# Optimization experiments

Hardware: AMD Instinct MI355X
Metric: run time of the kernel (lower is better)

The kernel has to match this reference:

```python
import jax, jax.numpy as jnp
import numpy as np

B, L, H, E = 8, 4096, 8, 64
NEIGH = 128          # neigh_size: local window length (entries per row of band mask)
SPLITS = 32          # number of Q blocks
L1 = L // SPLITS     # rows per block = 128 (neigh_size <= L/splits holds with equality)


def setup_inputs() -> dict:
    key = jax.random.key(0)
    kq, kk, kv = jax.random.split(key, 3)
    return {
        "queries": jax.random.normal(kq, (B, L, H, E), jnp.float32),
        "keys":    jax.random.normal(kk, (B, L, H, E), jnp.float32),
        "values":  jax.random.normal(kv, (B, L, H, E), jnp.float32),
    }


def reference(queries, keys, values):
    scale = 1.0 / np.sqrt(E)
    # Global key index of each entry in a KV block: block j covers [j*l1 - neigh, j*l1 + l1)
    kv_idx = (jnp.arange(SPLITS)[:, None] * L1
              + jnp.arange(L1 + NEIGH)[None, :] - NEIGH)      # [splits, l1+neigh]
    kv_gather = jnp.clip(kv_idx, 0, L - 1)                    # out-of-range entries get masked

    Qb = queries.reshape(B, SPLITS, L1, H, E)                 # [B, j, l, H, E]
    Kb = keys[:, kv_gather]                                   # [B, j, m, H, E]
    Vb = values[:, kv_gather]                                 # [B, j, m, H, E]

    scores = jnp.einsum('bjlhe,bjmhe->bhjlm', Qb, Kb) * scale # [B, H, splits, l1, l1+neigh]

    # Band: key global index k satisfies q - neigh < k <= q  <=>  l < m <= l + neigh
    l_idx = jnp.arange(L1)[:, None]
    m_idx = jnp.arange(L1 + NEIGH)[None, :]
    band = (m_idx > l_idx) & (m_idx <= l_idx + NEIGH)         # [l1, l1+neigh]
    valid = band[None, :, :] & (kv_idx[:, None, :] >= 0)      # [splits, l1, l1+neigh]

    scores = jnp.where(valid[None, None], scores, jnp.float32(-1e9))
    attn = jax.nn.softmax(scores, axis=-1)
    out = jnp.einsum('bhjlm,bjmhe->bjlhe', attn, Vb)          # [B, splits, l1, H, E]
    return out.reshape(B, L, H, E)
```

## Files before the change

kernel.cpp:

```cpp
#include <hip/hip_runtime.h>

#define B_ 8
#define L_ 4096
#define H_ 8
#define E_ 64
#define NEIGH_ 128
#define SPLITS_ 32
#define BQ 128
#define WIN 256
#define KPAD 72
#define NT 10
#define NP 5

typedef float f32x4 __attribute__((ext_vector_type(4)));
typedef __bf16 bf16x8 __attribute__((ext_vector_type(8)));
typedef unsigned short u16x4 __attribute__((ext_vector_type(4)));
typedef unsigned short u16x8 __attribute__((ext_vector_type(8)));
typedef unsigned int u32;

__device__ inline unsigned short f2bf(float f) {
  unsigned int u = __float_as_uint(f);
  u += 0x7fff + ((u >> 16) & 1);
  return (unsigned short)(u >> 16);
}
__device__ inline u32 pack2(float a, float b) {
  return (u32)f2bf(a) | ((u32)f2bf(b) << 16);
}

__global__ __launch_bounds__(512, 4) void la_kernel(
    const float* __restrict__ Q, const float* __restrict__ K,
    const float* __restrict__ V, float* __restrict__ out) {
  const int lid = blockIdx.x + SPLITS_ * (blockIdx.y + H_ * blockIdx.z);
  const int logical = (lid & 7) * 256 + (lid >> 3);
  const int j = logical & (SPLITS_ - 1);
  const int h = (logical >> 5) & (H_ - 1);
  const int b = logical >> 8;
  const int t = threadIdx.x;

  __shared__ unsigned short Ks[WIN * KPAD];
  __shared__ u32 Vs32[E_ * (WIN / 2)];

  const int q0 = j * BQ;
  const int g0 = q0 - NEIGH_;

  for (int i = 0; i < 8; ++i) {
    int idx = t + i * 512;
    int km = idx >> 4, c4 = idx & 15;
    int g = g0 + km; g = g < 0 ? 0 : g;
    const float4 v = *(const float4*)(K + ((((size_t)b * L_) + g) * H_ + h) * E_ + c4 * 4);
    u16x4 p = { f2bf(v.x), f2bf(v.y), f2bf(v.z), f2bf(v.w) };
    *(u16x4*)&Ks[km * KPAD + c4 * 4] = p;
  }
  for (int i = 0; i < 4; ++i) {
    int idx = t + i * 512;
    int kp = idx >> 4, c4 = idx & 15;
    int k0g = g0 + 2 * kp, k1g = k0g + 1;
    k0g = k0g < 0 ? 0 : k0g; k1g = k1g < 0 ? 0 : k1g;
    const float4 v0 = *(const float4*)(V + ((((size_t)b * L_) + k0g) * H_ + h) * E_ + c4 * 4);
    const float4 v1 = *(const float4*)(V + ((((size_t)b * L_) + k1g) * H_ + h) * E_ + c4 * 4);
    int g = kp >> 2;
    int ko = kp & 3;
    const float a0[4] = {v0.x, v0.y, v0.z, v0.w};
    const float a1[4] = {v1.x, v1.y, v1.z, v1.w};
#pragma unroll
    for (int w = 0; w < 4; ++w) {
      int e = c4 * 4 + w;
      int gs = g ^ (e & 31);
      Vs32[e * 128 + gs * 4 + ko] = pack2(a0[w], a1[w]);
    }
  }

  const int wv = t >> 6, lane = t & 63;
  const int l15 = lane & 15, quad = lane >> 4;
  const int r0 = wv * 16;
  const int lq = r0 + l15;
  const int start = wv & ~1;
  const int ks0 = start >> 1;

  bf16x8 qfrag[2];
  {
    const float* qrow = Q + ((((size_t)b * L_) + q0 + lq) * H_ + h) * E_;
#pragma unroll
    for (int ks = 0; ks < 2; ++ks) {
      const float4 x = *(const float4*)(qrow + ks * 32 + quad * 8);
      const float4 y = *(const float4*)(qrow + ks * 32 + quad * 8 + 4);
      u16x8 p = { f2bf(x.x), f2bf(x.y), f2bf(x.z), f2bf(x.w),
                  f2bf(y.x), f2bf(y.y), f2bf(y.z), f2bf(y.w) };
      qfrag[ks] = __builtin_bit_cast(bf16x8, p);
    }
  }
  __syncthreads();

  f32x4 S[NT];
#pragma unroll
  for (int si = 0; si < NT; ++si) S[si] = (f32x4){0.f, 0.f, 0.f, 0.f};
#pragma unroll
  for (int ks = 0; ks < 2; ++ks) {
#pragma unroll
    for (int si = 0; si < NT; ++si) {
      int kt = start + si;
      bf16x8 a = __builtin_bit_cast(bf16x8,
          *(const u16x8*)&Ks[(kt * 16 + l15) * KPAD + ks * 32 + quad * 8]);
      S[si] = __builtin_amdgcn_mfma_f32_16x16x32_bf16(a, qfrag[ks], S[si], 0, 0, 0);
    }
  }

  float m = -1e30f;
#pragma unroll
  for (int si = 0; si < NT; ++si) {
#pragma unroll
    for (int r = 0; r < 4; ++r) {
      int key = (start + si) * 16 + quad * 4 + r;
      float s = S[si][r] * 0.125f;
      bool valid = (key > lq) & (key <= lq + NEIGH_) & (g0 + key >= 0);
      s = valid ? s : -1e30f;
      S[si][r] = s;
      m = fmaxf(m, s);
    }
  }
  m = fmaxf(m, __shfl_xor(m, 16));
  m = fmaxf(m, __shfl_xor(m, 32));

  float lsum = 0.f;
  u32 pk[NT][2];
#pragma unroll
  for (int si = 0; si < NT; ++si) {
    float p0 = __expf(S[si][0] - m);
    float p1 = __expf(S[si][1] - m);
    float p2 = __expf(S[si][2] - m);
    float p3 = __expf(S[si][3] - m);
    lsum += (p0 + p1) + (p2 + p3);
    pk[si][0] = pack2(p0, p1);
    pk[si][1] = pack2(p2, p3);
  }
  lsum += __shfl_xor(lsum, 16);
  lsum += __shfl_xor(lsum, 32);
  const float inv = 1.0f / lsum;

  f32x4 O[4];
#pragma unroll
  for (int et = 0; et < 4; ++et) O[et] = (f32x4){0.f, 0.f, 0.f, 0.f};
  const int srcBase = 16 * ((quad & 1) * 2) + l15;
  const bool hiTile = (quad >> 1) != 0;
#pragma unroll
  for (int pi = 0; pi < NP; ++pi) {
    const int ap = ks0 + pi;
    u32 a32[4];
#pragma unroll
    for (int k = 0; k < 4; ++k) {
      int src = srcBase + 16 * (k >> 1);
      u32 u0 = (u32)__shfl((int)pk[2 * pi][k & 1], src);
      u32 u1 = (u32)__shfl((int)pk[2 * pi + 1][k & 1], src);
      a32[k] = hiTile ? u1 : u0;
    }
    bf16x8 afrag = __builtin_bit_cast(bf16x8,
        (u32 __attribute__((ext_vector_type(4)))){a32[0], a32[1], a32[2], a32[3]});
#pragma unroll
    for (int et = 0; et < 4; ++et) {
      int e = et * 16 + l15;
      int gs = (ap * 4 + quad) ^ (e & 31);
      bf16x8 bfrag = __builtin_bit_cast(bf16x8,
          *(const u16x8*)((const unsigned short*)Vs32 + e * 256 + gs * 8));
      O[et] = __builtin_amdgcn_mfma_f32_16x16x32_bf16(afrag, bfrag, O[et], 0, 0, 0);
    }
  }

  float invq[4];
#pragma unroll
  for (int r = 0; r < 4; ++r) invq[r] = __shfl(inv, quad * 4 + r);
#pragma unroll
  for (int et = 0; et < 4; ++et)
#pragma unroll
    for (int r = 0; r < 4; ++r) {
      int row = r0 + quad * 4 + r;
      out[((((size_t)b * L_) + q0 + row) * H_ + h) * E_ + et * 16 + l15] = O[et][r] * invq[r];
    }
}

extern "C" void kernel_launch(void* const* d_in, const int* in_sizes, int n_in,
                              void* d_out, int out_size, void* d_ws, size_t ws_size,
                              hipStream_t stream) {
  const float* q = (const float*)d_in[0];
  const float* k = (const float*)d_in[1];
  const float* v = (const float*)d_in[2];
  float* o = (float*)d_out;
  dim3 grid(SPLITS_, H_, B_);
  la_kernel<<<grid, 512, 0, stream>>>(q, k, v, o);
}
```

Before: 226.1 us.

## Load K fragments directly from global memory and drop K shared-memory staging

K is no longer staged in LDS. Each wave loads its own K rows from global memory straight into MFMA fragments, which removes the K LDS write/read and moves the barrier to after the softmax so the V staging overlaps with QK compute. It also switches to native bf16 conversion intrinsics, raises the launch-bounds occupancy hint from 4 to 6, and raises wave priority around the PV MFMAs. In exchange, K is read redundantly from global (overlapping windows across waves, via L2) and register pressure may spill under the tighter launch bound.

```diff
diff --git a/kernel.cpp b/kernel.cpp
--- a/kernel.cpp
+++ b/kernel.cpp
@@ -8,26 +8,27 @@
 #define SPLITS_ 32
 #define BQ 128
 #define WIN 256
-#define KPAD 72
 #define NT 10
 #define NP 5
 
 typedef float f32x4 __attribute__((ext_vector_type(4)));
+typedef __bf16 bf16x2 __attribute__((ext_vector_type(2)));
 typedef __bf16 bf16x8 __attribute__((ext_vector_type(8)));
-typedef unsigned short u16x4 __attribute__((ext_vector_type(4)));
 typedef unsigned short u16x8 __attribute__((ext_vector_type(8)));
 typedef unsigned int u32;
+typedef u32 u32x4 __attribute__((ext_vector_type(4)));
 
-__device__ inline unsigned short f2bf(float f) {
-  unsigned int u = __float_as_uint(f);
-  u += 0x7fff + ((u >> 16) & 1);
-  return (unsigned short)(u >> 16);
+__device__ inline u32 pack2(float a, float b) {
+  bf16x2 t = {(__bf16)a, (__bf16)b};
+  return __builtin_bit_cast(u32, t);
 }
-__device__ inline u32 pack2(float a, float b) {
-  return (u32)f2bf(a) | ((u32)f2bf(b) << 16);
+__device__ inline bf16x8 cvt8(const float4& x, const float4& y) {
+  bf16x8 r = {(__bf16)x.x, (__bf16)x.y, (__bf16)x.z, (__bf16)x.w,
+              (__bf16)y.x, (__bf16)y.y, (__bf16)y.z, (__bf16)y.w};
+  return r;
 }
 
-__global__ __launch_bounds__(512, 4) void la_kernel(
+__global__ __launch_bounds__(512, 6) void la_kernel(
     const float* __restrict__ Q, const float* __restrict__ K,
     const float* __restrict__ V, float* __restrict__ out) {
   const int lid = blockIdx.x + SPLITS_ * (blockIdx.y + H_ * blockIdx.z);
@@ -37,20 +38,11 @@
   const int b = logical >> 8;
   const int t = threadIdx.x;
 
-  __shared__ unsigned short Ks[WIN * KPAD];
   __shared__ u32 Vs32[E_ * (WIN / 2)];
 
   const int q0 = j * BQ;
   const int g0 = q0 - NEIGH_;
 
-  for (int i = 0; i < 8; ++i) {
-    int idx = t + i * 512;
-    int km = idx >> 4, c4 = idx & 15;
-    int g = g0 + km; g = g < 0 ? 0 : g;
-    const float4 v = *(const float4*)(K + ((((size_t)b * L_) + g) * H_ + h) * E_ + c4 * 4);
-    u16x4 p = { f2bf(v.x), f2bf(v.y), f2bf(v.z), f2bf(v.w) };
-    *(u16x4*)&Ks[km * KPAD + c4 * 4] = p;
-  }
   for (int i = 0; i < 4; ++i) {
     int idx = t + i * 512;
     int kp = idx >> 4, c4 = idx & 15;
@@ -84,25 +76,24 @@
     for (int ks = 0; ks < 2; ++ks) {
       const float4 x = *(const float4*)(qrow + ks * 32 + quad * 8);
       const float4 y = *(const float4*)(qrow + ks * 32 + quad * 8 + 4);
-      u16x8 p = { f2bf(x.x), f2bf(x.y), f2bf(x.z), f2bf(x.w),
-                  f2bf(y.x), f2bf(y.y), f2bf(y.z), f2bf(y.w) };
-      qfrag[ks] = __builtin_bit_cast(bf16x8, p);
+      qfrag[ks] = cvt8(x, y);
     }
   }
-  __syncthreads();
 
   f32x4 S[NT];
 #pragma unroll
   for (int si = 0; si < NT; ++si) S[si] = (f32x4){0.f, 0.f, 0.f, 0.f};
 #pragma unroll
-  for (int ks = 0; ks < 2; ++ks) {
-#pragma unroll
-    for (int si = 0; si < NT; ++si) {
-      int kt = start + si;
-      bf16x8 a = __builtin_bit_cast(bf16x8,
-          *(const u16x8*)&Ks[(kt * 16 + l15) * KPAD + ks * 32 + quad * 8]);
-      S[si] = __builtin_amdgcn_mfma_f32_16x16x32_bf16(a, qfrag[ks], S[si], 0, 0, 0);
-    }
+  for (int si = 0; si < NT; ++si) {
+    int g = g0 + (start + si) * 16 + l15;
+    g = g < 0 ? 0 : g;
+    const float* krow = K + ((((size_t)b * L_) + g) * H_ + h) * E_;
+    const float4 x0 = *(const float4*)(krow + quad * 8);
+    const float4 y0 = *(const float4*)(krow + quad * 8 + 4);
+    const float4 x1 = *(const float4*)(krow + 32 + quad * 8);
+    const float4 y1 = *(const float4*)(krow + 32 + quad * 8 + 4);
+    S[si] = __builtin_amdgcn_mfma_f32_16x16x32_bf16(cvt8(x0, y0), qfrag[0], S[si], 0, 0, 0);
+    S[si] = __builtin_amdgcn_mfma_f32_16x16x32_bf16(cvt8(x1, y1), qfrag[1], S[si], 0, 0, 0);
   }
 
   float m = -1e30f;
@@ -137,6 +128,8 @@
   lsum += __shfl_xor(lsum, 32);
   const float inv = 1.0f / lsum;
 
+  __syncthreads();
+
   f32x4 O[4];
 #pragma unroll
   for (int et = 0; et < 4; ++et) O[et] = (f32x4){0.f, 0.f, 0.f, 0.f};
@@ -154,7 +147,8 @@
       a32[k] = hiTile ? u1 : u0;
     }
     bf16x8 afrag = __builtin_bit_cast(bf16x8,
-        (u32 __attribute__((ext_vector_type(4)))){a32[0], a32[1], a32[2], a32[3]});
+        (u32x4){a32[0], a32[1], a32[2], a32[3]});
+    __builtin_amdgcn_s_setprio(1);
 #pragma unroll
     for (int et = 0; et < 4; ++et) {
       int e = et * 16 + l15;
@@ -163,6 +157,7 @@
           *(const u16x8*)((const unsigned short*)Vs32 + e * 256 + gs * 8));
       O[et] = __builtin_amdgcn_mfma_f32_16x16x32_bf16(afrag, bfrag, O[et], 0, 0, 0);
     }
+    __builtin_amdgcn_s_setprio(0);
   }
 
   float invq[4];
```

Result: slower. 263.1 us (+16.4%).

## Alias K and V shared buffers, defer V staging, fold scale into Q

Applied to the files above, without the earlier changes.

K and V now share one shared-memory buffer, so V is loaded and transposed into LDS only after the QK^T and softmax phase, with extra barriers between the phases. The aim is to halve LDS use per block, letting launch bounds target 6 blocks per CU instead of 4. The softmax scale and log2(e) are folded into Q before the bf16 conversion so the softmax can use exp2 without a per-score multiply, and the band-mask test is simplified. Conversions use native bf16 casts, and setprio is raised around the PV MFMAs. The trade-off is that the V global loads are serialized after the score phase, and the higher occupancy target may cause register spills.

```diff
diff --git a/kernel.cpp b/kernel.cpp
--- a/kernel.cpp
+++ b/kernel.cpp
@@ -11,23 +11,22 @@
 #define KPAD 72
 #define NT 10
 #define NP 5
+#define SCALE_LOG2E 0.18033688011112042f
 
 typedef float f32x4 __attribute__((ext_vector_type(4)));
+typedef __bf16 bf16x2 __attribute__((ext_vector_type(2)));
 typedef __bf16 bf16x8 __attribute__((ext_vector_type(8)));
-typedef unsigned short u16x4 __attribute__((ext_vector_type(4)));
 typedef unsigned short u16x8 __attribute__((ext_vector_type(8)));
 typedef unsigned int u32;
-
-__device__ inline unsigned short f2bf(float f) {
-  unsigned int u = __float_as_uint(f);
-  u += 0x7fff + ((u >> 16) & 1);
-  return (unsigned short)(u >> 16);
+typedef u32 u32x2 __attribute__((ext_vector_type(2)));
+typedef u32 u32x4 __attribute__((ext_vector_type(4)));
+
+__device__ inline u32 pack2(float a, float b) {
+  bf16x2 t = {(__bf16)a, (__bf16)b};
+  return __builtin_bit_cast(u32, t);
 }
-__device__ inline u32 pack2(float a, float b) {
-  return (u32)f2bf(a) | ((u32)f2bf(b) << 16);
-}
-
-__global__ __launch_bounds__(512, 4) void la_kernel(
+
+__global__ __launch_bounds__(512, 6) void la_kernel(
     const float* __restrict__ Q, const float* __restrict__ K,
     const float* __restrict__ V, float* __restrict__ out) {
   const int lid = blockIdx.x + SPLITS_ * (blockIdx.y + H_ * blockIdx.z);
@@ -37,37 +36,20 @@
   const int b = logical >> 8;
   const int t = threadIdx.x;
 
-  __shared__ unsigned short Ks[WIN * KPAD];
-  __shared__ u32 Vs32[E_ * (WIN / 2)];
+  __shared__ __align__(16) unsigned char smem[WIN * KPAD * 2];
+  unsigned short* Ks = (unsigned short*)smem;
+  u32* Vs32 = (u32*)smem;
 
   const int q0 = j * BQ;
   const int g0 = q0 - NEIGH_;
 
+#pragma unroll
   for (int i = 0; i < 8; ++i) {
     int idx = t + i * 512;
     int km = idx >> 4, c4 = idx & 15;
     int g = g0 + km; g = g < 0 ? 0 : g;
     const float4 v = *(const float4*)(K + ((((size_t)b * L_) + g) * H_ + h) * E_ + c4 * 4);
-    u16x4 p = { f2bf(v.x), f2bf(v.y), f2bf(v.z), f2bf(v.w) };
-    *(u16x4*)&Ks[km * KPAD + c4 * 4] = p;
-  }
-  for (int i = 0; i < 4; ++i) {
-    int idx = t + i * 512;
-    int kp = idx >> 4, c4 = idx & 15;
-    int k0g = g0 + 2 * kp, k1g = k0g + 1;
-    k0g = k0g < 0 ? 0 : k0g; k1g = k1g < 0 ? 0 : k1g;
-    const float4 v0 = *(const float4*)(V + ((((size_t)b * L_) + k0g) * H_ + h) * E_ + c4 * 4);
-    const float4 v1 = *(const float4*)(V + ((((size_t)b * L_) + k1g) * H_ + h) * E_ + c4 * 4);
-    int g = kp >> 2;
-    int ko = kp & 3;
-    const float a0[4] = {v0.x, v0.y, v0.z, v0.w};
-    const float a1[4] = {v1.x, v1.y, v1.z, v1.w};
-#pragma unroll
-    for (int w = 0; w < 4; ++w) {
-      int e = c4 * 4 + w;
-      int gs = g ^ (e & 31);
-      Vs32[e * 128 + gs * 4 + ko] = pack2(a0[w], a1[w]);
-    }
+    *(u32x2*)&Ks[km * KPAD + c4 * 4] = (u32x2){pack2(v.x, v.y), pack2(v.z, v.w)};
   }
 
   const int wv = t >> 6, lane = t & 63;
@@ -84,9 +66,11 @@
     for (int ks = 0; ks < 2; ++ks) {
       const float4 x = *(const float4*)(qrow + ks * 32 + quad * 8);
       const float4 y = *(const float4*)(qrow + ks * 32 + quad * 8 + 4);
-      u16x8 p = { f2bf(x.x), f2bf(x.y), f2bf(x.z), f2bf(x.w),
-                  f2bf(y.x), f2bf(y.y), f2bf(y.z), f2bf(y.w) };
-      qfrag[ks] = __builtin_bit_cast(bf16x8, p);
+      bf16x8 r = {(__bf16)(x.x * SCALE_LOG2E), (__bf16)(x.y * SCALE_LOG2E),
+                  (__bf16)(x.z * SCALE_LOG2E), (__bf16)(x.w * SCALE_LOG2E),
+                  (__bf16)(y.x * SCALE_LOG2E), (__bf16)(y.y * SCALE_LOG2E),
+                  (__bf16)(y.z * SCALE_LOG2E), (__bf16)(y.w * SCALE_LOG2E)};
+      qfrag[ks] = r;
     }
   }
   __syncthreads();
@@ -105,15 +89,15 @@
     }
   }
 
+  const int minkey = (j == 0) ? NEIGH_ : 0;
   float m = -1e30f;
 #pragma unroll
   for (int si = 0; si < NT; ++si) {
 #pragma unroll
     for (int r = 0; r < 4; ++r) {
       int key = (start + si) * 16 + quad * 4 + r;
-      float s = S[si][r] * 0.125f;
-      bool valid = (key > lq) & (key <= lq + NEIGH_) & (g0 + key >= 0);
-      s = valid ? s : -1e30f;
+      bool valid = ((u32)(key - lq - 1) < 128u) & (key >= minkey);
+      float s = valid ? S[si][r] : -1e30f;
       S[si][r] = s;
       m = fmaxf(m, s);
     }
@@ -125,10 +109,10 @@
   u32 pk[NT][2];
 #pragma unroll
   for (int si = 0; si < NT; ++si) {
-    float p0 = __expf(S[si][0] - m);
-    float p1 = __expf(S[si][1] - m);
-    float p2 = __expf(S[si][2] - m);
-    float p3 = __expf(S[si][3] - m);
+    float p0 = exp2f(S[si][0] - m);
+    float p1 = exp2f(S[si][1] - m);
+    float p2 = exp2f(S[si][2] - m);
+    float p3 = exp2f(S[si][3] - m);
     lsum += (p0 + p1) + (p2 + p3);
     pk[si][0] = pack2(p0, p1);
     pk[si][1] = pack2(p2, p3);
@@ -136,6 +120,36 @@
   lsum += __shfl_xor(lsum, 16);
   lsum += __shfl_xor(lsum, 32);
   const float inv = 1.0f / lsum;
+
+  float4 vA[4], vB[4];
+#pragma unroll
+  for (int i = 0; i < 4; ++i) {
+    int idx = t + i * 512;
+    int kp = idx >> 4, c4 = idx & 15;
+    int k0g = g0 + 2 * kp, k1g = k0g + 1;
+    k0g = k0g < 0 ? 0 : k0g; k1g = k1g < 0 ? 0 : k1g;
+    vA[i] = *(const float4*)(V + ((((size_t)b * L_) + k0g) * H_ + h) * E_ + c4 * 4);
+    vB[i] = *(const float4*)(V + ((((size_t)b * L_) + k1g) * H_ + h) * E_ + c4 * 4);
+  }
+
+  __syncthreads();
+
+#pragma unroll
+  for (int i = 0; i < 4; ++i) {
+    int idx = t + i * 512;
+    int kp = idx >> 4, c4 = idx & 15;
+    int g = kp >> 2;
+    int ko = kp & 3;
+    const float a0[4] = {vA[i].x, vA[i].y, vA[i].z, vA[i].w};
+    const float a1[4] = {vB[i].x, vB[i].y, vB[i].z, vB[i].w};
+#pragma unroll
+    for (int w = 0; w < 4; ++w) {
+      int e = c4 * 4 + w;
+      int gs = g ^ (e & 31);
+      Vs32[e * 128 + gs * 4 + ko] = pack2(a0[w], a1[w]);
+    }
+  }
+  __syncthreads();
 
   f32x4 O[4];
 #pragma unroll
@@ -154,7 +168,8 @@
       a32[k] = hiTile ? u1 : u0;
     }
     bf16x8 afrag = __builtin_bit_cast(bf16x8,
-        (u32 __attribute__((ext_vector_type(4)))){a32[0], a32[1], a32[2], a32[3]});
+        (u32x4){a32[0], a32[1], a32[2], a32[3]});
+    __builtin_amdgcn_s_setprio(1);
 #pragma unroll
     for (int et = 0; et < 4; ++et) {
       int e = et * 16 + l15;
@@ -163,6 +178,7 @@
           *(const u16x8*)((const unsigned short*)Vs32 + e * 256 + gs * 8));
       O[et] = __builtin_amdgcn_mfma_f32_16x16x32_bf16(afrag, bfrag, O[et], 0, 0, 0);
     }
+    __builtin_amdgcn_s_setprio(0);
   }
 
   float invq[4];
```

After: 223.8 us. No clear change (-1.0%).
